# Optimization experiments

Measured on AMD Instinct MI355X. Metric: run time of the kernel, lower is better.

## Reference

```python
import jax, jax.numpy as jnp
import numpy as np

N_NODES = 50000
N_EDGES = 800000
CH = 128
N_GRAPHS = 8
ADD_TO_EDGE_SCORE = 0.5


def edge_scores(x, row, col, lin_w, lin_b, n):
    """Raw edge score via Linear([x_row||x_col]) then scatter-softmax over col."""
    C = x.shape[1]
    # split-weight form of cat([x[row], x[col]]) @ W^T + b (avoids the [E,2C] concat)
    raw = x[row] @ lin_w[0, :C] + x[col] @ lin_w[0, C:] + lin_b[0]  # [E]
    mx = jax.ops.segment_max(raw, col, num_segments=n)
    ex = jnp.exp(raw - mx[col])
    den = jax.ops.segment_sum(ex, col, num_segments=n)
    return ex / (den[col] + 1e-16) + ADD_TO_EDGE_SCORE


def greedy_match_cluster(row_np, col_np, score_np, n):
    """Greedy maximal matching in descending-score order + 2-element clustering."""
    perm = np.argsort(-score_np)
    rows = row_np.tolist()
    cols = col_np.tolist()
    used = np.zeros(n, dtype=bool)
    match = np.zeros(len(rows), dtype=bool)
    for e in perm.tolist():
        r = rows[e]
        c = cols[e]
        if not (used[r] or used[c]):
            match[e] = True
            used[r] = True
            used[c] = True
    cluster = np.arange(n)
    cluster[col_np[match]] = row_np[match]
    _, cluster = np.unique(cluster, return_inverse=True)
    return match, cluster


def setup_inputs() -> dict:
    key = jax.random.key(0)
    k1, k2, k3, k4, k5 = jax.random.split(key, 5)
    x = jax.random.normal(k1, (N_NODES, CH), dtype=jnp.float32)
    edge_index = jax.random.randint(k2, (2, N_EDGES), 0, N_NODES)
    batch = jnp.sort(jax.random.randint(k3, (N_NODES,), 0, N_GRAPHS))
    bound = 1.0 / np.sqrt(2 * CH)
    lin_w = jax.random.uniform(k4, (1, 2 * CH), minval=-bound, maxval=bound, dtype=jnp.float32)
    lin_b = jax.random.uniform(k5, (1,), minval=-bound, maxval=bound, dtype=jnp.float32)
    return {"x": x, "edge_index": edge_index, "batch": batch, "lin_w": lin_w, "lin_b": lin_b}


def reference(x, edge_index, batch, lin_w, lin_b):
    n = x.shape[0]
    row, col = edge_index[0], edge_index[1]
    score = edge_scores(x, row, col, lin_w, lin_b, n)  # [E]

    # sequential greedy matching / cluster relabeling (host side, non-differentiable)
    row_np, col_np = np.asarray(row), np.asarray(col)
    match, cluster_np = greedy_match_cluster(row_np, col_np, np.asarray(score), n)
    c = int(cluster_np.max()) + 1
    match_idx = jnp.asarray(np.nonzero(match)[0])
    cluster = jnp.asarray(cluster_np, dtype=jnp.int32)

    # pooled features scaled by the contracted edge's score (1.0 for singletons)
    new_x = jax.ops.segment_sum(x, cluster, num_segments=c)  # [c, C]
    root = cluster[row[match_idx]]
    new_edge_score = jnp.ones((c,), x.dtype).at[root].set(score[match_idx])
    new_x = new_x * new_edge_score[:, None]

    # coalesce(cluster[edge_index]): sort + dedup
    lin_idx = cluster_np[row_np].astype(np.int64) * c + cluster_np[col_np]
    uniq = np.unique(lin_idx)
    new_edge_index = jnp.asarray(np.stack([uniq // c, uniq % c]).astype(np.int32))

    new_batch = jnp.zeros((c,), dtype=batch.dtype).at[cluster].set(batch)
    return new_x, new_edge_index, new_batch, new_edge_score, cluster
```

## Files before the change

### kernel.cpp

```cpp
#include <hip/hip_runtime.h>

typedef unsigned int u32;
typedef unsigned short u16;
typedef unsigned long long u64;

#define CH_ 128

__device__ __forceinline__ u32 f2ord(float f){
  u32 u = __float_as_uint(f);
  return ((int)u < 0) ? ~u : (u | 0x80000000u);
}
__device__ __forceinline__ float ord2f(u32 u){
  return (u & 0x80000000u) ? __uint_as_float(u & 0x7FFFFFFFu) : __uint_as_float(~u);
}
__device__ __forceinline__ u32 ldu32(const u32* p){
  return __hip_atomic_load(p, __ATOMIC_RELAXED, __HIP_MEMORY_SCOPE_AGENT);
}
__device__ __forceinline__ void stu32(u32* p, u32 v){
  __hip_atomic_store(p, v, __ATOMIC_RELAXED, __HIP_MEMORY_SCOPE_AGENT);
}

__global__ void k_init(u32* hdr, u32* mxbits, double* den, u64* sw,
                       int* craw, int* medge, u32* deg, u32* acur,
                       u32* wpos, u32* offarr, u32 ucap, int N, int E){
  int i0 = blockIdx.x*blockDim.x + threadIdx.x;
  int nt = gridDim.x*blockDim.x;
  for (int v = i0; v < N; v += nt){
    mxbits[v]=0u; den[v]=0.0; sw[v]=0ull; craw[v]=v; medge[v]=-1;
    deg[v]=0u; acur[v]=0u; wpos[v]=0u;
    if (ucap) offarr[v] = (u32)v * ucap;
  }
  if (i0 == 0){
    for (int i = 0; i < 64; i++) hdr[i] = 0u;
    hdr[6] = (u32)N;
    offarr[N] = ucap ? (u32)N*ucap : (u32)(2*E);
  }
}

__global__ void k_dots(const float* __restrict__ x, const float* __restrict__ lw,
                       float* __restrict__ s, float* __restrict__ t, int N){
  int wid = threadIdx.x >> 6, lane = threadIdx.x & 63;
  int node = blockIdx.x*4 + wid;
  if (node >= N) return;
  const float* xr = x + (size_t)node*CH_;
  float xa = xr[lane], xb = xr[64+lane];
  float sv = xa*lw[lane]      + xb*lw[64+lane];
  float tv = xa*lw[128+lane]  + xb*lw[192+lane];
  #pragma unroll
  for (int m = 1; m < 64; m <<= 1){ sv += __shfl_xor(sv, m); tv += __shfl_xor(tv, m); }
  if (lane == 0){ s[node]=sv; t[node]=tv; }
}

__global__ void k_rawmax(const float* __restrict__ s, const float* __restrict__ t,
                         const int* __restrict__ row, const int* __restrict__ col,
                         const float* __restrict__ lb, float* __restrict__ rawex,
                         u32* __restrict__ mxbits, u32* __restrict__ rc,
                         u32* __restrict__ deg, u32 ucap, int E){
  float b = lb[0];
  int i0 = blockIdx.x*blockDim.x + threadIdx.x;
  int nt = gridDim.x*blockDim.x;
  for (int e = i0; e < E; e += nt){
    int r = row[e], c = col[e];
    float raw = (s[r] + t[c]) + b;
    rawex[e] = raw;
    atomicMax(&mxbits[c], f2ord(raw));
    rc[e] = ((u32)r << 16) | (u32)c;
    if (!ucap){
      atomicAdd(&deg[r], 1u);
      atomicAdd(&deg[c], 1u);
    }
  }
}

__global__ void k_exden(const int* __restrict__ col, const u32* __restrict__ mxbits,
                        float* __restrict__ rawex, double* __restrict__ den, int E){
  int i0 = blockIdx.x*blockDim.x + threadIdx.x;
  int nt = gridDim.x*blockDim.x;
  for (int e = i0; e < E; e += nt){
    int c = col[e];
    float ex = expf(rawex[e] - ord2f(mxbits[c]));
    rawex[e] = ex;
    atomicAdd(&den[c], (double)ex);
  }
}

__global__ void scan_p1(const u32* __restrict__ in, u32* __restrict__ out,
                        u32* __restrict__ bsums, const u32* __restrict__ nptr){
  __shared__ u32 sh[256];
  u32 n = *nptr;
  int t = threadIdx.x;
  u32 i = blockIdx.x*256u + (u32)t;
  u32 v = (i < n) ? in[i] : 0u;
  sh[t] = v; __syncthreads();
  for (int o = 1; o < 256; o <<= 1){
    u32 a = (t >= o) ? sh[t-o] : 0u;
    __syncthreads();
    sh[t] += a;
    __syncthreads();
  }
  if (i < n) out[i] = sh[t] - v;
  if (t == 255) bsums[blockIdx.x] = sh[255];
}
__global__ void scan_p2(u32* bsums, u32* total){
  __shared__ u32 sh[256];
  int t = threadIdx.x;
  u32 v = bsums[t];
  sh[t] = v; __syncthreads();
  for (int o = 1; o < 256; o <<= 1){
    u32 a = (t >= o) ? sh[t-o] : 0u;
    __syncthreads();
    sh[t] += a;
    __syncthreads();
  }
  bsums[t] = sh[t] - v;
  if (t == 255 && total) *total = sh[255];
}
__global__ void scan_p3(u32* out, const u32* __restrict__ bsums, const u32* __restrict__ nptr){
  u32 n = *nptr;
  u32 i = blockIdx.x*256u + threadIdx.x;
  if (i < n) out[i] += bsums[blockIdx.x];
}

__global__ void k_scoreadj(const u32* __restrict__ rc, const float* __restrict__ rawex,
                           float* __restrict__ score, const double* __restrict__ den,
                           const u32* __restrict__ offarr, u32* __restrict__ acur,
                           u64* __restrict__ adj, u16* __restrict__ adjp,
                           u32 ucap, int P, int E, int N){
  int i0 = blockIdx.x*blockDim.x + threadIdx.x;
  int nt = gridDim.x*blockDim.x;
  u32 span = ((u32)N + P - 1) / P;
  for (int p = 0; p < P; p++){
    u32 vlo = (u32)p * span;
    u32 vhi = vlo + span; if (vhi > (u32)N) vhi = (u32)N;
    for (int e = i0; e < E; e += nt){
      u32 pk = rc[e]; u32 r = pk >> 16, c = pk & 0xFFFFu;
      bool wr = (r >= vlo) & (r < vhi);
      bool wc = (c >= vlo) & (c < vhi);
      if (p == 0 || wr || wc){
        float sc = rawex[e]/(float)den[c] + 0.5f;
        if (p == 0) score[e] = sc;
        u64 k = ((u64)__float_as_uint(sc) << 20) | (u64)(0xFFFFFu - (u32)e);
        if (wr){
          u32 slot = atomicAdd(&acur[r], 1u);
          if (!ucap || slot < ucap){
            u32 pr = offarr[r] + slot;
            adj[pr] = k; adjp[pr] = (u16)c;
          }
        }
        if (wc){
          u32 slot = atomicAdd(&acur[c], 1u);
          if (!ucap || slot < ucap){
            u32 pc = offarr[c] + slot;
            adj[pc] = k; adjp[pc] = (u16)r;
          }
        }
      }
    }
  }
}

__global__ void k_adjsort(const u32* __restrict__ offarr, const u32* __restrict__ acur,
                          u64* __restrict__ adj, u16* __restrict__ adjp,
                          u32 ucap, int N){
  __shared__ u64 shk[512];
  __shared__ u32 shp[512];
  int lane = threadIdx.x;
  u32 capn = ucap ? ucap : 0xFFFFFFFFu;
  for (int seg = blockIdx.x; seg < N; seg += gridDim.x){
    u32 base = offarr[seg];
    u32 cnt = acur[seg]; if (cnt > capn) cnt = capn;
    int n = (int)cnt;
    if (n <= 1) continue;
    if (n <= 64){
      u64 v = (lane < n) ? adj[base + lane] : 0ull;
      u32 pr = (lane < n) ? (u32)adjp[base + lane] : 0u;
      #pragma unroll
      for (int k2 = 2; k2 <= 64; k2 <<= 1)
        for (int j = k2 >> 1; j > 0; j >>= 1){
          u64 pv = __shfl_xor(v, j);
          u32 pp = (u32)__shfl_xor((int)pr, j);
          bool up  = ((lane & k2) == 0);
          bool low = ((lane & j) == 0);
          bool take_mx = (up == low);
          bool swap = take_mx ? (pv > v) : (pv < v);
          if (swap){ v = pv; pr = pp; }
        }
      if (lane < n){ adj[base + lane] = v; adjp[base + lane] = (u16)pr; }
    } else {
      int msz = 128; while (msz < n) msz <<= 1;
      for (int i = lane; i < msz; i += 64){
        shk[i] = (i < n) ? adj[base + i] : 0ull;
        shp[i] = (i < n) ? (u32)adjp[base + i] : 0u;
      }
      __syncthreads();
      for (int k2 = 2; k2 <= msz; k2 <<= 1){
        for (int j = k2 >> 1; j > 0; j >>= 1){
          for (int i = lane; i < msz; i += 64){
            int ix = i ^ j;
            if (ix > i){
              u64 a = shk[i], b2 = shk[ix];
              bool desc = ((i & k2) == 0);
              if (desc ? (a < b2) : (a > b2)){
                shk[i] = b2; shk[ix] = a;
                u32 t2 = shp[i]; shp[i] = shp[ix]; shp[ix] = t2;
              }
            }
          }
          __syncthreads();
        }
      }
      for (int i = lane; i < n; i += 64){ adj[base+i] = shk[i]; adjp[base+i] = (u16)shp[i]; }
      __syncthreads();
    }
  }
}

__global__ void k_suitor(const u32* __restrict__ rc, const u32* __restrict__ offarr,
                         const u32* __restrict__ acur,
                         const u64* __restrict__ adj, const u16* __restrict__ adjp,
                         u64* sw, u32* wpos, u32 ucap, int N){
  int i0 = blockIdx.x*blockDim.x + threadIdx.x;
  int nt = gridDim.x*blockDim.x;
  u32 capn = ucap ? ucap : 0xFFFFFFFFu;
  for (int v0 = i0; v0 < N; v0 += nt){
    u32 u = (u32)v0;
    u32 pos = offarr[u];
    u32 cnt = acur[u]; if (cnt > capn) cnt = capn;
    u32 end = pos + cnt;
    while (pos < end){
      u64 k = adj[pos];
      u32 v = (u32)adjp[pos];
      pos++;
      if (sw[v] >= k) continue;
      stu32(&wpos[u], pos);
      u64 old = atomicMax((unsigned long long*)&sw[v], (unsigned long long)k);
      if (old >= k) continue;
      if (old == 0ull) break;
      u32 e2 = 0xFFFFFu - (u32)(old & 0xFFFFFu);
      u32 p2 = rc[e2];
      u = ((p2 >> 16) == v) ? (p2 & 0xFFFFu) : (p2 >> 16);
      u32 st = offarr[u];
      u32 c2 = acur[u]; if (c2 > capn) c2 = capn;
      end = st + c2;
      u32 wp = ldu32(&wpos[u]);
      pos = (wp > st) ? wp : st;
    }
  }
}

__global__ void k_exroot(const u64* __restrict__ sw, const u32* __restrict__ rc,
                         int* __restrict__ craw, int* __restrict__ medge,
                         u32* __restrict__ rf, int N){
  int v = blockIdx.x*blockDim.x + threadIdx.x;
  if (v >= N) return;
  u64 k = sw[v];
  bool iscol = false;
  if (k != 0ull){
    u32 e = 0xFFFFFu - (u32)(k & 0xFFFFFu);
    u32 p = rc[e]; u32 r = p >> 16, c = p & 0xFFFFu;
    if ((u32)v == c && sw[r] == k){
      craw[c] = (int)r; medge[r] = (int)e;
      iscol = (r != c);
    }
  }
  rf[v] = iscol ? 0u : 1u;
}

__global__ void k_clusterzero(const int* __restrict__ craw, const u32* __restrict__ newid,
                              int* __restrict__ clout, float* __restrict__ out, size_t offC,
                              u32* __restrict__ hist, u32* __restrict__ cur2,
                              u32* __restrict__ uniqcnt, int N, int M){
  int i = blockIdx.x*blockDim.x + threadIdx.x;
  if (i < M){ hist[i]=0u; cur2[i]=0u; uniqcnt[i]=0u; }
  if (i < N){
    int cl = (int)newid[craw[i]];
    clout[i] = cl;
    out[offC + i] = (float)cl;
  }
}

__global__ void k_hist(const int* __restrict__ row, const int* __restrict__ clout,
                       u32* __restrict__ hist, int E){
  int i0 = blockIdx.x*blockDim.x + threadIdx.x;
  int nt = gridDim.x*blockDim.x;
  for (int e = i0; e < E; e += nt) atomicAdd(&hist[clout[row[e]]], 1u);
}

__global__ void k_scatter(const int* __restrict__ row, const int* __restrict__ col,
                          const int* __restrict__ clout, const u32* __restrict__ segoff,
                          u32* __restrict__ cur2, u32* __restrict__ ccbuf,
                          const u32* __restrict__ hdr, int E){
  const int P = 4;
  int cnum = (int)hdr[2];
  int span = (cnum + P - 1) / P;
  int i0 = blockIdx.x*blockDim.x + threadIdx.x;
  int nt = gridDim.x*blockDim.x;
  for (int p = 0; p < P; p++){
    int lo = p*span;
    int hi = lo + span; if (hi > cnum) hi = cnum;
    for (int e = i0; e < E; e += nt){
      int cr = clout[row[e]];
      if (cr < lo || cr >= hi) continue;
      u32 pos = segoff[cr] + atomicAdd(&cur2[cr], 1u);
      ccbuf[pos] = (u32)clout[col[e]];
    }
  }
}

__global__ void k_segsort(const u32* __restrict__ hdr, const u32* __restrict__ hist,
                          const u32* __restrict__ segoff, u32* __restrict__ ccbuf,
                          u32* __restrict__ uniqcnt){
  int c = (int)hdr[2];
  __shared__ u32 sh[1024];
  int lane = threadIdx.x;
  for (int seg = blockIdx.x; seg < c; seg += gridDim.x){
    int n = (int)hist[seg];
    if (n <= 0){ if (lane == 0) uniqcnt[seg] = 0u; continue; }
    u32 off = segoff[seg];
    if (n <= 64){
      u32 v = (lane < n) ? ccbuf[off + lane] : 0xFFFFFFFFu;
      #pragma unroll
      for (int k = 2; k <= 64; k <<= 1)
        for (int j = k >> 1; j > 0; j >>= 1){
          u32 p = __shfl_xor(v, j);
          bool up  = ((lane & k) == 0);
          bool low = ((lane & j) == 0);
          u32 mn = v < p ? v : p, mx = v < p ? p : v;
          v = (up == low) ? mn : mx;
        }
      u32 pv = __shfl_up(v, 1);
      bool un = (lane < n) && (lane == 0 || v != pv);
      u64 bal = __ballot(un);
      int cnt = __popcll(bal);
      int rk  = __popcll(bal & ((1ull << lane) - 1ull));
      if (un) ccbuf[off + rk] = v;
      if (lane == 0) uniqcnt[seg] = (u32)cnt;
    } else {
      int nn = n > 1024 ? 1024 : n;
      for (int i = lane; i < nn; i += 64) sh[i] = ccbuf[off + i];
      __syncthreads();
      for (int p = 0; p < nn; p++){
        int st = p & 1;
        for (int i = lane; 2*i + 1 + st < nn; i += 64){
          int a = 2*i + st;
          u32 x0 = sh[a], x1 = sh[a+1];
          if (x0 > x1){ sh[a] = x1; sh[a+1] = x0; }
        }
        __syncthreads();
      }
      if (lane == 0){
        int cnt = 0; u32 prev = 0u;
        for (int i = 0; i < nn; i++){
          u32 xv = sh[i];
          if (i == 0 || xv != prev){ ccbuf[off + cnt] = xv; cnt++; prev = xv; }
        }
        uniqcnt[seg] = (u32)cnt;
      }
      __syncthreads();
    }
  }
}

__global__ void k_out(const u32* __restrict__ hdr, const u32* __restrict__ segoff,
                      const u32* __restrict__ uniqcnt, const u32* __restrict__ uniqoff,
                      const u32* __restrict__ ccbuf, const int* __restrict__ craw,
                      const u32* __restrict__ newid, const int* __restrict__ medge,
                      const int* __restrict__ row, const int* __restrict__ col,
                      const float* __restrict__ score, const int* __restrict__ batch,
                      const float* __restrict__ x, float* __restrict__ out, int N){
  int c = (int)hdr[2]; u32 Ep = hdr[3];
  size_t base = (size_t)c * CH_;
  size_t offB = base + 2ull * (size_t)Ep;
  size_t offS = offB + (size_t)c;
  int gw   = (blockIdx.x*blockDim.x + threadIdx.x) >> 6;
  int lane = threadIdx.x & 63;
  int nw   = (gridDim.x*blockDim.x) >> 6;
  for (int seg = gw; seg < c; seg += nw){
    int cnt = (int)uniqcnt[seg];
    u32 so = segoff[seg], uo = uniqoff[seg];
    for (int j = lane; j < cnt; j += 64){
      u32 cc = ccbuf[so + j];
      out[base + uo + j]              = (float)seg;
      out[base + (size_t)Ep + uo + j] = (float)cc;
    }
  }
  for (int i = gw; i < N; i += nw){
    if (craw[i] != i) continue;
    int j = (int)newid[i];
    int e = medge[i];
    int lo = i, hi = i; float sc = 1.0f;
    if (e >= 0){
      int r = row[e], cc = col[e];
      lo = min(r, cc); hi = max(r, cc);
      sc = score[e];
    }
    float v0 = x[(size_t)lo*CH_ + lane];
    float v1 = x[(size_t)lo*CH_ + 64 + lane];
    if (hi != lo){ v0 += x[(size_t)hi*CH_ + lane]; v1 += x[(size_t)hi*CH_ + 64 + lane]; }
    out[(size_t)j*CH_ + lane]      = v0 * sc;
    out[(size_t)j*CH_ + 64 + lane] = v1 * sc;
    if (lane == 0){
      out[offB + j] = (float)batch[hi];
      out[offS + j] = sc;
    }
  }
}

extern "C" void kernel_launch(void* const* d_in, const int* in_sizes, int n_in,
                              void* d_out, int out_size, void* d_ws, size_t ws_size,
                              hipStream_t stream) {
  const float* x     = (const float*)d_in[0];
  const int*   eidx  = (const int*)d_in[1];
  const int*   batch = (const int*)d_in[2];
  const float* lw    = (const float*)d_in[3];
  const float* lb    = (const float*)d_in[4];

  int N = in_sizes[0] / CH_;
  int E = in_sizes[1] / 2;
  const int* row = eidx;
  const int* col = eidx + E;
  float* out = (float*)d_out;

  char* w = (char*)d_ws;
  size_t off = 0;
  auto carve = [&](size_t bytes) -> void* {
    void* p = w + off;
    off += (bytes + 255) & ~(size_t)255;
    return p;
  };
  u32*    hdr    = (u32*)   carve(256);
  double* den    = (double*)carve((size_t)N*8);
  u64*    sw     = (u64*)   carve((size_t)N*8);
  float*  s      = (float*) carve((size_t)N*4);
  float*  t      = (float*) carve((size_t)N*4);
  float*  rawex  = (float*) carve((size_t)E*4);
  float*  score  = (float*) carve((size_t)E*4);
  u32*    mxbits = (u32*)   carve((size_t)N*4);
  int*    craw   = (int*)   carve((size_t)N*4);
  u32*    rf     = (u32*)   carve((size_t)N*4);
  u32*    newid  = (u32*)   carve((size_t)N*4);
  int*    medge  = (int*)   carve((size_t)N*4);
  int*    clout  = (int*)   carve((size_t)N*4);
  u32*    rc     = (u32*)   carve((size_t)E*4);
  u32*    deg    = (u32*)   carve((size_t)N*4);
  u32*    acur   = (u32*)   carve((size_t)N*4);
  u32*    wpos   = (u32*)   carve((size_t)N*4);
  u32*    offarr = (u32*)   carve((size_t)(N+1)*4);
  u32*    bsums  = (u32*)   carve(256*4);

  u32 cap = 80;
  size_t adjp_b_bytes = ((size_t)N*cap*2 + 255) & ~(size_t)255;
  size_t adj_b_bytes  = ((size_t)N*cap*8 + 255) & ~(size_t)255;
  size_t adjp_c_bytes = ((size_t)(2*(size_t)E)*2 + 255) & ~(size_t)255;
  size_t adj_c_bytes  = ((size_t)(2*(size_t)E)*8 + 255) & ~(size_t)255;
  bool buckets = (off + adjp_b_bytes + adj_b_bytes + (1u<<20) <= ws_size);
  u16* adjp; u64* adj;
  if (buckets){
    adjp = (u16*)carve((size_t)N*cap*2);
    adj  = (u64*)carve((size_t)N*cap*8);
  } else {
    cap = 0;
    adjp = (u16*)carve((size_t)(2*(size_t)E)*2);
    adj  = (u64*)carve((size_t)(2*(size_t)E)*8);
  }
  (void)adjp_c_bytes; (void)adj_c_bytes;
  char* a = (char*)adj;
  size_t aoff = 0;
  auto acarve = [&](size_t bytes) -> void* {
    void* p = a + aoff;
    aoff += (bytes + 255) & ~(size_t)255;
    return p;
  };
  u32* ccbuf   = (u32*)acarve((size_t)E*4);
  u32* hist    = (u32*)acarve((size_t)(N+64)*4);
  u32* segoff  = (u32*)acarve((size_t)(N+64)*4);
  u32* cur2    = (u32*)acarve((size_t)(N+64)*4);
  u32* uniqcnt = (u32*)acarve((size_t)(N+64)*4);
  u32* uniqoff = (u32*)acarve((size_t)(N+64)*4);
  (void)n_in;

  int nbE = (E + 255) / 256;
  int nbN = (N + 255) / 256;
  int P_adj = buckets ? 16 : 8;

  k_init<<<512, 256, 0, stream>>>(hdr, mxbits, den, sw, craw, medge, deg, acur,
                                  wpos, offarr, cap, N, E);
  k_dots<<<(N + 3)/4, 256, 0, stream>>>(x, lw, s, t, N);
  k_rawmax<<<nbE, 256, 0, stream>>>(s, t, row, col, lb, rawex, mxbits, rc, deg, cap, E);
  k_exden<<<nbE, 256, 0, stream>>>(col, mxbits, rawex, den, E);

  if (!buckets){
    scan_p1<<<256, 256, 0, stream>>>(deg, offarr, bsums, &hdr[6]);
    scan_p2<<<1, 256, 0, stream>>>(bsums, &hdr[7]);
    scan_p3<<<256, 256, 0, stream>>>(offarr, bsums, &hdr[6]);
  }

  k_scoreadj<<<nbE, 256, 0, stream>>>(rc, rawex, score, den, offarr, acur, adj, adjp,
                                      cap, P_adj, E, N);
  k_adjsort<<<4096, 64, 0, stream>>>(offarr, acur, adj, adjp, cap, N);
  k_suitor<<<nbN, 256, 0, stream>>>(rc, offarr, acur, adj, adjp, sw, wpos, cap, N);
  k_exroot<<<nbN, 256, 0, stream>>>(sw, rc, craw, medge, rf, N);

  scan_p1<<<256, 256, 0, stream>>>(rf, newid, bsums, &hdr[6]);
  scan_p2<<<1, 256, 0, stream>>>(bsums, &hdr[2]);
  scan_p3<<<256, 256, 0, stream>>>(newid, bsums, &hdr[6]);

  k_clusterzero<<<(N + 64 + 255)/256, 256, 0, stream>>>(craw, newid, clout, out,
                                                        (size_t)(out_size - N),
                                                        hist, cur2, uniqcnt, N, N + 64);
  k_hist<<<nbE, 256, 0, stream>>>(row, clout, hist, E);

  scan_p1<<<256, 256, 0, stream>>>(hist, segoff, bsums, &hdr[2]);
  scan_p2<<<1, 256, 0, stream>>>(bsums, &hdr[4]);
  scan_p3<<<256, 256, 0, stream>>>(segoff, bsums, &hdr[2]);

  k_scatter<<<nbE, 256, 0, stream>>>(row, col, clout, segoff, cur2, ccbuf, hdr, E);
  k_segsort<<<4096, 64, 0, stream>>>(hdr, hist, segoff, ccbuf, uniqcnt);

  scan_p1<<<256, 256, 0, stream>>>(uniqcnt, uniqoff, bsums, &hdr[2]);
  scan_p2<<<1, 256, 0, stream>>>(bsums, &hdr[3]);
  scan_p3<<<256, 256, 0, stream>>>(uniqoff, bsums, &hdr[2]);

  k_out<<<4096, 256, 0, stream>>>(hdr, segoff, uniqcnt, uniqoff, ccbuf, craw, newid,
                                  medge, row, col, score, batch, x, out, N);
}
```

Before: 471.3 us.

## Partition adjacency build by XCD vertex range and precompute scores in place

The final score computation moves into a separate k_score kernel that overwrites rawex in place, which removes the separate score buffer. The adjacency-build kernel no longer loops sequentially over P vertex partitions across the whole grid. Instead each block handles one edge chunk for one of 8 vertex ranges, chosen by blockIdx&7 to line up with the MI355X XCDs, so the atomics and scattered writes for a vertex range stay within one XCD's L2. This adds one extra pass over the edges, and it relies on the hardware assigning blocks round-robin across XCDs.

```diff
diff --git a/kernel.cpp b/kernel.cpp
--- a/kernel.cpp
+++ b/kernel.cpp
@@ -82,6 +82,14 @@
     rawex[e] = ex;
     atomicAdd(&den[c], (double)ex);
   }
+}
+
+__global__ void k_score(const int* __restrict__ col, float* __restrict__ rawex,
+                        const double* __restrict__ den, int E){
+  int i0 = blockIdx.x*blockDim.x + threadIdx.x;
+  int nt = gridDim.x*blockDim.x;
+  for (int e = i0; e < E; e += nt)
+    rawex[e] = rawex[e]/(float)den[col[e]] + 0.5f;
 }
 
 __global__ void scan_p1(const u32* __restrict__ in, u32* __restrict__ out,
@@ -121,38 +129,37 @@
   if (i < n) out[i] += bsums[blockIdx.x];
 }
 
-__global__ void k_scoreadj(const u32* __restrict__ rc, const float* __restrict__ rawex,
-                           float* __restrict__ score, const double* __restrict__ den,
-                           const u32* __restrict__ offarr, u32* __restrict__ acur,
-                           u64* __restrict__ adj, u16* __restrict__ adjp,
-                           u32 ucap, int P, int E, int N){
-  int i0 = blockIdx.x*blockDim.x + threadIdx.x;
-  int nt = gridDim.x*blockDim.x;
-  u32 span = ((u32)N + P - 1) / P;
-  for (int p = 0; p < P; p++){
-    u32 vlo = (u32)p * span;
-    u32 vhi = vlo + span; if (vhi > (u32)N) vhi = (u32)N;
-    for (int e = i0; e < E; e += nt){
-      u32 pk = rc[e]; u32 r = pk >> 16, c = pk & 0xFFFFu;
-      bool wr = (r >= vlo) & (r < vhi);
-      bool wc = (c >= vlo) & (c < vhi);
-      if (p == 0 || wr || wc){
-        float sc = rawex[e]/(float)den[c] + 0.5f;
-        if (p == 0) score[e] = sc;
-        u64 k = ((u64)__float_as_uint(sc) << 20) | (u64)(0xFFFFFu - (u32)e);
-        if (wr){
-          u32 slot = atomicAdd(&acur[r], 1u);
-          if (!ucap || slot < ucap){
-            u32 pr = offarr[r] + slot;
-            adj[pr] = k; adjp[pr] = (u16)c;
-          }
-        }
-        if (wc){
-          u32 slot = atomicAdd(&acur[c], 1u);
-          if (!ucap || slot < ucap){
-            u32 pc = offarr[c] + slot;
-            adj[pc] = k; adjp[pc] = (u16)r;
-          }
+__global__ void __launch_bounds__(256)
+k_scoreadj(const u32* __restrict__ rc, const float* __restrict__ score,
+           const u32* __restrict__ offarr, u32* __restrict__ acur,
+           u64* __restrict__ adj, u16* __restrict__ adjp,
+           u32 ucap, int ce, int E, int N){
+  int xcd   = blockIdx.x & 7;
+  int chunk = blockIdx.x >> 3;
+  int vspan = (N + 7) >> 3;
+  int vlo = xcd * vspan;
+  int vhi = vlo + vspan; if (vhi > N) vhi = N;
+  int ebeg = chunk * ce;
+  int eend = ebeg + ce; if (eend > E) eend = E;
+  for (int e = ebeg + threadIdx.x; e < eend; e += blockDim.x){
+    u32 pk = rc[e];
+    int r = (int)(pk >> 16), c = (int)(pk & 0xFFFFu);
+    bool wr = (r >= vlo) & (r < vhi);
+    bool wc = (c >= vlo) & (c < vhi);
+    if (wr | wc){
+      u64 k = ((u64)__float_as_uint(score[e]) << 20) | (u64)(0xFFFFFu - (u32)e);
+      if (wr){
+        u32 slot = atomicAdd(&acur[r], 1u);
+        if (!ucap || slot < ucap){
+          u32 pr = offarr[r] + slot;
+          adj[pr] = k; adjp[pr] = (u16)c;
+        }
+      }
+      if (wc){
+        u32 slot = atomicAdd(&acur[c], 1u);
+        if (!ucap || slot < ucap){
+          u32 pc = offarr[c] + slot;
+          adj[pc] = k; adjp[pc] = (u16)r;
         }
       }
     }
@@ -434,7 +441,6 @@
   float*  s      = (float*) carve((size_t)N*4);
   float*  t      = (float*) carve((size_t)N*4);
   float*  rawex  = (float*) carve((size_t)E*4);
-  float*  score  = (float*) carve((size_t)E*4);
   u32*    mxbits = (u32*)   carve((size_t)N*4);
   int*    craw   = (int*)   carve((size_t)N*4);
   u32*    rf     = (u32*)   carve((size_t)N*4);
@@ -451,8 +457,6 @@
   u32 cap = 80;
   size_t adjp_b_bytes = ((size_t)N*cap*2 + 255) & ~(size_t)255;
   size_t adj_b_bytes  = ((size_t)N*cap*8 + 255) & ~(size_t)255;
-  size_t adjp_c_bytes = ((size_t)(2*(size_t)E)*2 + 255) & ~(size_t)255;
-  size_t adj_c_bytes  = ((size_t)(2*(size_t)E)*8 + 255) & ~(size_t)255;
   bool buckets = (off + adjp_b_bytes + adj_b_bytes + (1u<<20) <= ws_size);
   u16* adjp; u64* adj;
   if (buckets){
@@ -463,7 +467,6 @@
     adjp = (u16*)carve((size_t)(2*(size_t)E)*2);
     adj  = (u64*)carve((size_t)(2*(size_t)E)*8);
   }
-  (void)adjp_c_bytes; (void)adj_c_bytes;
   char* a = (char*)adj;
   size_t aoff = 0;
   auto acarve = [&](size_t bytes) -> void* {
@@ -481,13 +484,15 @@
 
   int nbE = (E + 255) / 256;
   int nbN = (N + 255) / 256;
-  int P_adj = buckets ? 16 : 8;
+  int ce  = 4096;
+  int kch = (E + ce - 1) / ce;
 
   k_init<<<512, 256, 0, stream>>>(hdr, mxbits, den, sw, craw, medge, deg, acur,
                                   wpos, offarr, cap, N, E);
   k_dots<<<(N + 3)/4, 256, 0, stream>>>(x, lw, s, t, N);
   k_rawmax<<<nbE, 256, 0, stream>>>(s, t, row, col, lb, rawex, mxbits, rc, deg, cap, E);
   k_exden<<<nbE, 256, 0, stream>>>(col, mxbits, rawex, den, E);
+  k_score<<<nbE, 256, 0, stream>>>(col, rawex, den, E);
 
   if (!buckets){
     scan_p1<<<256, 256, 0, stream>>>(deg, offarr, bsums, &hdr[6]);
@@ -495,8 +500,8 @@
     scan_p3<<<256, 256, 0, stream>>>(offarr, bsums, &hdr[6]);
   }
 
-  k_scoreadj<<<nbE, 256, 0, stream>>>(rc, rawex, score, den, offarr, acur, adj, adjp,
-                                      cap, P_adj, E, N);
+  k_scoreadj<<<8*kch, 256, 0, stream>>>(rc, rawex, offarr, acur, adj, adjp,
+                                        cap, ce, E, N);
   k_adjsort<<<4096, 64, 0, stream>>>(offarr, acur, adj, adjp, cap, N);
   k_suitor<<<nbN, 256, 0, stream>>>(rc, offarr, acur, adj, adjp, sw, wpos, cap, N);
   k_exroot<<<nbN, 256, 0, stream>>>(sw, rc, craw, medge, rf, N);
@@ -522,5 +527,5 @@
   scan_p3<<<256, 256, 0, stream>>>(uniqoff, bsums, &hdr[2]);
 
   k_out<<<4096, 256, 0, stream>>>(hdr, segoff, uniqcnt, uniqoff, ccbuf, craw, newid,
-                                  medge, row, col, score, batch, x, out, N);
-}
+                                  medge, row, col, rawex, batch, x, out, N);
+}
```

After: 447.6 us. 5.0% less time.
